# Kernel tuning notes

Hardware: AMD Instinct MI355X
Metric: run time of the kernel (lower is better)

The kernel has to match this reference:

```python
import jax, jax.numpy as jnp
import numpy as np

B, T, C, H, O = 256, 256, 32, 512, 32
OUT_TIME = 32


def setup_inputs() -> dict:
    key = jax.random.key(0)
    ks = jax.random.split(key, 10)
    times = jnp.arange(T, dtype=jnp.float32)
    coeffs = jax.random.normal(ks[0], (B, T, C), jnp.float32)
    final_index = jax.random.randint(ks[1], (B,), 0, T)
    dW = jax.random.normal(ks[2], (T - 1, B, H), jnp.float32)  # unit-normal; scaled by sqrt(dt) inside
    s = lambda k, shape, fan: jax.random.normal(k, shape, jnp.float32) / np.float32(np.sqrt(fan))
    return {
        "times": times, "coeffs": coeffs, "final_index": final_index, "dW": dW,
        "W_init": s(ks[3], (C, H), C), "b_init": jnp.zeros((H,), jnp.float32),
        "W1": s(ks[4], (H + C, H), H + C), "b1": jnp.zeros((H,), jnp.float32),
        "W2": s(ks[5], (H, H), H), "b2": jnp.zeros((H,), jnp.float32),
        "Wg": s(ks[6], (H, H), H), "bg": jnp.zeros((H,), jnp.float32),
        "Wh1": s(ks[7], (H, H), H), "bh1": jnp.zeros((H,), jnp.float32),
        "Wh2": s(ks[8], (H, O), H), "bh2": jnp.zeros((O,), jnp.float32),
    }


def reference(times, coeffs, final_index, dW, W_init, b_init, W1, b1, W2, b2, Wg, bg, Wh1, bh1, Wh2, bh2):
    # dt = max(min(diff(times)), 0.001)  (Euler method default in the torch module)
    dt = jnp.maximum(jnp.min(times[1:] - times[:-1]), jnp.float32(0.001))
    sqdt = jnp.sqrt(dt)

    x_seq = jnp.transpose(coeffs, (1, 0, 2))  # [T, B, C] control path at grid points
    # z0 = initial_network(X.evaluate(times[0]))
    z0 = x_seq[0] @ W_init + b_init  # [B, H]

    def step(y, inp):
        xk, dWk = inp  # [B, C], [B, H]
        h = jnp.tanh(jnp.concatenate([y, xk], axis=-1) @ W1 + b1)
        f = jnp.tanh(h @ W2 + b2)                # drift
        g = jax.nn.sigmoid(y @ Wg + bg)          # diagonal diffusion
        y_next = y + f * dt + g * (sqdt * dWk)   # Euler-Maruyama step
        return y_next, y_next

    _, zs = jax.lax.scan(step, z0, (x_seq[:-1], dW))  # zs: [T-1, B, H]
    z = jnp.concatenate([z0[None], zs], axis=0)       # [T, B, H]
    z = jnp.transpose(z, (1, 0, 2))                   # [B, T, H]  (transpose loop in torch code)
    z_tail = z[:, z.shape[1] - OUT_TIME:, :]          # last output_time steps
    return jax.nn.relu(z_tail @ Wh1 + bh1) @ Wh2 + bh2  # [B, OUT_TIME, O]
```

## Files before the change

kernel.cpp:

```cpp
#include <hip/hip_runtime.h>
#include <stdint.h>
#include <stddef.h>

typedef __attribute__((ext_vector_type(8))) short short8;
typedef __attribute__((ext_vector_type(8))) _Float16 half8;
typedef __attribute__((ext_vector_type(4))) float f32x4;
typedef unsigned long long ull;

#define T_  256
#define B_  256
#define C_  32
#define H_  512
#define O_  32
#define KB1 17
#define NT1 64
#define KB2 16
#define NT2 32

__device__ __forceinline__ short f2h(float f) {
  _Float16 h = (_Float16)f;
  return __builtin_bit_cast(short, h);
}
__device__ __forceinline__ void f2hl(float f, short& hi, short& lo) {
  _Float16 h = (_Float16)f;
  _Float16 l = (_Float16)(f - (float)h);
  hi = __builtin_bit_cast(short, h);
  lo = __builtin_bit_cast(short, l);
}
__device__ __forceinline__ unsigned int pack_hl(float f) {
  short h, l;
  f2hl(f, h, l);
  return (unsigned int)(unsigned short)h | ((unsigned int)(unsigned short)l << 16);
}
__device__ __forceinline__ float fast_tanh(float x) {
  float e = __expf(2.0f * x);
  return 1.0f - 2.0f / (e + 1.0f);
}
__device__ __forceinline__ float fast_sigmoid(float x) {
  return 1.0f / (1.0f + __expf(-x));
}
__device__ __forceinline__ f32x4 mfma16(half8 a, half8 b, f32x4 c) {
  return __builtin_amdgcn_mfma_f32_16x16x32_f16(a, b, c, 0, 0, 0);
}
__device__ __forceinline__ half8 ld8(const short* p) { return *(const half8*)p; }

__device__ __forceinline__ void st_coh(unsigned int* p, unsigned int v) {
  __hip_atomic_store(p, v, __ATOMIC_RELAXED, __HIP_MEMORY_SCOPE_AGENT);
}
__device__ __forceinline__ ull ld_coh(const ull* p) {
  return __hip_atomic_load(p, __ATOMIC_RELAXED, __HIP_MEMORY_SCOPE_AGENT);
}

__device__ __forceinline__ void stage_pl(const ull* src, short* hi, short* lo,
                                         int stride, int tid) {
  ull v[16];
  #pragma unroll
  for (int i = 0; i < 8; ++i) {
    int p = i * 256 + tid;
    v[2 * i]     = ld_coh(src + 2 * p);
    v[2 * i + 1] = ld_coh(src + 2 * p + 1);
  }
  #pragma unroll
  for (int i = 0; i < 8; ++i) {
    int p = i * 256 + tid;
    int row = p >> 7, col4 = (p & 127) << 2;
    unsigned int u0 = (unsigned int)v[2 * i],     u1 = (unsigned int)(v[2 * i] >> 32);
    unsigned int u2 = (unsigned int)v[2 * i + 1], u3 = (unsigned int)(v[2 * i + 1] >> 32);
    unsigned int hiA = (u0 & 0xffffu) | (u1 << 16);
    unsigned int hiB = (u2 & 0xffffu) | (u3 << 16);
    unsigned int loA = (u0 >> 16) | (u1 & 0xffff0000u);
    unsigned int loB = (u2 >> 16) | (u3 & 0xffff0000u);
    *(ull*)(hi + row * stride + col4) = (ull)hiA | ((ull)hiB << 32);
    *(ull*)(lo + row * stride + col4) = (ull)loA | ((ull)loB << 32);
  }
}

__device__ __forceinline__ void bg_barrier(unsigned int* cnt, unsigned int target) {
  __syncthreads();
  if (threadIdx.x == 0) {
    __hip_atomic_fetch_add(cnt, 1u, __ATOMIC_RELAXED, __HIP_MEMORY_SCOPE_AGENT);
    while (__hip_atomic_load(cnt, __ATOMIC_RELAXED, __HIP_MEMORY_SCOPE_AGENT) < target)
      __builtin_amdgcn_s_sleep(1);
  }
  __syncthreads();
}

__global__ void pack_b1s(const float* __restrict__ W1, const float* __restrict__ Wg,
                         short* __restrict__ hi, short* __restrict__ lo) {
  int gid = blockIdx.x * 256 + threadIdx.x;
  if (gid >= KB1 * NT1 * 512) return;
  int j = gid & 7, lane = (gid >> 3) & 63, tile = gid >> 9;
  int nt = tile % NT1, kb = tile / NT1;
  int k = kb * 32 + ((lane >> 4) << 3) + j;
  int n = ((nt & 31) << 4) + (lane & 15);
  float v = 0.f;
  if (nt < 32)      v = W1[k * H_ + n];
  else if (k < H_)  v = Wg[k * H_ + n];
  short h, l;
  f2hl(v, h, l);
  hi[gid] = h; lo[gid] = l;
}

__global__ void pack_s(const float* __restrict__ src, short* __restrict__ hi,
                       short* __restrict__ lo, int Ksrc, int Nsrc, int KB, int NT) {
  int gid = blockIdx.x * 256 + threadIdx.x;
  if (gid >= KB * NT * 512) return;
  int j = gid & 7, lane = (gid >> 3) & 63, tile = gid >> 9;
  int nt = tile % NT, kb = tile / NT;
  int k = kb * 32 + ((lane >> 4) << 3) + j;
  int n = (nt << 4) + (lane & 15);
  float v = (k < Ksrc && n < Nsrc) ? src[k * Nsrc + n] : 0.f;
  short h, l;
  f2hl(v, h, l);
  hi[gid] = h;
  if (lo) lo[gid] = l;
}

__global__ __launch_bounds__(256, 1) void sde_kernel(
    const float* __restrict__ times, const float* __restrict__ coeffs,
    const float* __restrict__ dW,
    const float* __restrict__ b_init, const float* __restrict__ b1,
    const float* __restrict__ b2, const float* __restrict__ bgb,
    const short* __restrict__ B1h, const short* __restrict__ B1l,
    const short* __restrict__ W2h, const short* __restrict__ W2l,
    const short* __restrict__ WIh, const short* __restrict__ WIl,
    unsigned int* __restrict__ y_pk, unsigned int* __restrict__ h_pk,
    short* __restrict__ zt, unsigned int* __restrict__ cnt_base) {
  __shared__ short yx_hi[16][552];
  __shared__ short yx_lo[16][552];
  __shared__ short hh_hi[16][520];
  __shared__ short hh_lo[16][520];
  __shared__ float g_x[16][32];
  __shared__ float redbuf[4];

  const int tid = threadIdx.x;
  const int w = tid >> 6, l = tid & 63;
  const int ra = l & 15, kq = l >> 4;
  const int bid = blockIdx.x;
  const int bg = bid & 15, cg = bid >> 4;
  const int R0 = bg << 4;
  unsigned int* cnt = cnt_base + bg * 32;

  const int nt1w = (w < 2) ? (2 * cg + w) : (32 + 2 * cg + (w - 2));
  const int extcol = nt1w * 16 + ra;
  const int ntF = 2 * cg + (w & 1);
  const int fcol = ntF * 16 + ra;

  float d = 1e30f;
  if (tid < T_ - 1) d = times[tid + 1] - times[tid];
  #pragma unroll
  for (int s = 32; s >= 1; s >>= 1) d = fminf(d, __shfl_xor(d, s, 64));
  if (l == 0) redbuf[w] = d;

  half8 wb1h[17], wb1l[17];
  #pragma unroll
  for (int kb = 0; kb < 17; ++kb) {
    const size_t off = ((size_t)(kb * 64 + nt1w) << 9) + (l << 3);
    wb1h[kb] = ld8(B1h + off);
    wb1l[kb] = ld8(B1l + off);
  }
  half8 ww2h[16], ww2l[16];
  if (w < 2) {
    #pragma unroll
    for (int kb = 0; kb < 16; ++kb) {
      const size_t off = ((size_t)(kb * 32 + ntF) << 9) + (l << 3);
      ww2h[kb] = ld8(W2h + off);
      ww2l[kb] = ld8(W2l + off);
    }
  }

  if (tid < 64) {
    int row = tid >> 2, cc = (tid & 3) << 3;
    const float* xb = coeffs + (size_t)(R0 + row) * (T_ * C_) + cc;
    short8 hi, lo;
    #pragma unroll
    for (int j = 0; j < 8; ++j) {
      short h, l2;
      f2hl(xb[j], h, l2);
      hi[j] = h; lo[j] = l2;
    }
    *(short8*)&yx_hi[row][512 + cc] = hi;
    *(short8*)&yx_lo[row][512 + cc] = lo;
  }
  __syncthreads();
  float m = fminf(fminf(redbuf[0], redbuf[1]), fminf(redbuf[2], redbuf[3]));
  const float dt = fmaxf(m, 0.001f);
  const float sq = sqrtf(dt);

  const float b1v = (w < 2) ? b1[extcol] : 0.f;
  const float bgv = (w >= 2) ? bgb[extcol - 512] : 0.f;
  const float b2v = (w < 2) ? b2[fcol] : 0.f;

  float yr[4] = {0.f, 0.f, 0.f, 0.f};
  if (w < 2) {
    half8 ah = ld8(&yx_hi[ra][512 + (kq << 3)]);
    half8 al = ld8(&yx_lo[ra][512 + (kq << 3)]);
    half8 bh = ld8(WIh + ((size_t)ntF << 9) + (l << 3));
    half8 bl = ld8(WIl + ((size_t)ntF << 9) + (l << 3));
    f32x4 Z = {0.f, 0.f, 0.f, 0.f};
    Z = mfma16(ah, bh, Z); Z = mfma16(al, bh, Z); Z = mfma16(ah, bl, Z);
    float bi = b_init[fcol];
    #pragma unroll
    for (int r = 0; r < 4; ++r) {
      yr[r] = Z[r] + bi;
      st_coh(&y_pk[(size_t)(R0 + (kq << 2) + r) * H_ + fcol], pack_hl(yr[r]));
    }
  }
  bg_barrier(cnt, 16u);

  for (int k = 0; k < T_ - 1; ++k) {
    float dwv[4];
    if (w < 2) {
      const float* dwb = dW + ((size_t)k * B_ + R0) * H_ + fcol;
      #pragma unroll
      for (int r = 0; r < 4; ++r)
        dwv[r] = __builtin_nontemporal_load(dwb + ((kq << 2) + r) * H_);
    }
    stage_pl((const ull*)y_pk + R0 * 256, &yx_hi[0][0], &yx_lo[0][0], 552, tid);
    __syncthreads();
    f32x4 Aa = {0.f, 0.f, 0.f, 0.f}, Ab = Aa, Ac = Aa;
    #pragma unroll
    for (int kb = 0; kb < 17; ++kb) {
      half8 ah = ld8(&yx_hi[ra][(kb << 5) + (kq << 3)]);
      half8 al = ld8(&yx_lo[ra][(kb << 5) + (kq << 3)]);
      Aa = mfma16(ah, wb1h[kb], Aa);
      Ab = mfma16(al, wb1h[kb], Ab);
      Ac = mfma16(ah, wb1l[kb], Ac);
    }
    if (w < 2) {
      #pragma unroll
      for (int r = 0; r < 4; ++r) {
        float h = fast_tanh((Aa[r] + Ab[r]) + Ac[r] + b1v);
        st_coh(&h_pk[(size_t)(R0 + (kq << 2) + r) * H_ + extcol], pack_hl(h));
      }
    } else {
      #pragma unroll
      for (int r = 0; r < 4; ++r)
        g_x[(kq << 2) + r][((w - 2) << 4) + ra] =
            fast_sigmoid((Aa[r] + Ab[r]) + Ac[r] + bgv);
    }
    bg_barrier(cnt, 16u * (2u * (unsigned)k + 2u));
    stage_pl((const ull*)h_pk + R0 * 256, &hh_hi[0][0], &hh_lo[0][0], 520, tid);
    __syncthreads();
    if (w < 2) {
      f32x4 Fa = {0.f, 0.f, 0.f, 0.f}, Fb = Fa, Fc = Fa;
      #pragma unroll
      for (int kb = 0; kb < 16; ++kb) {
        half8 ah = ld8(&hh_hi[ra][(kb << 5) + (kq << 3)]);
        half8 al = ld8(&hh_lo[ra][(kb << 5) + (kq << 3)]);
        Fa = mfma16(ah, ww2h[kb], Fa);
        Fb = mfma16(al, ww2h[kb], Fb);
        Fc = mfma16(ah, ww2l[kb], Fc);
      }
      #pragma unroll
      for (int r = 0; r < 4; ++r) {
        float f = fast_tanh((Fa[r] + Fb[r]) + Fc[r] + b2v);
        float g = g_x[(kq << 2) + r][((w & 1) << 4) + ra];
        yr[r] += f * dt + g * (sq * dwv[r]);
        st_coh(&y_pk[(size_t)(R0 + (kq << 2) + r) * H_ + fcol], pack_hl(yr[r]));
      }
      if (k >= T_ - 1 - O_) {
        int t = k - (T_ - 1 - O_);
        #pragma unroll
        for (int r = 0; r < 4; ++r)
          zt[((size_t)(R0 + (kq << 2) + r) * O_ + t) * H_ + fcol] = f2h(yr[r]);
      }
    } else if (w == 2 && k < T_ - 2) {
      int row = l >> 2, cc = (l & 3) << 3;
      const float* xb =
          coeffs + (size_t)(R0 + row) * (T_ * C_) + (size_t)(k + 1) * C_ + cc;
      short8 hi, lo;
      #pragma unroll
      for (int j = 0; j < 8; ++j) {
        short h, l2;
        f2hl(xb[j], h, l2);
        hi[j] = h; lo[j] = l2;
      }
      *(short8*)&yx_hi[row][512 + cc] = hi;
      *(short8*)&yx_lo[row][512 + cc] = lo;
    }
    bg_barrier(cnt, 16u * (2u * (unsigned)k + 3u));
  }
}

__global__ __launch_bounds__(256) void head_kernel(
    const short* __restrict__ zt, const short* __restrict__ Wh1p,
    const short* __restrict__ Wh2p, const float* __restrict__ bh1,
    const float* __restrict__ bh2, float* __restrict__ out) {
  __shared__ short a_lds[32][520];
  __shared__ short h2_lds[32][520];
  const int tid = threadIdx.x;
  const int w = tid >> 6, l = tid & 63;
  const int ra = l & 15, kq = l >> 4;
  const int r0 = blockIdx.x << 5;

  const short* zb = zt + (size_t)r0 * H_;
  #pragma unroll
  for (int i = 0; i < 8; ++i) {
    int cidx = i * 256 + tid;
    int row = cidx >> 6, cc = (cidx & 63) << 3;
    *(short8*)&a_lds[row][cc] = *(const short8*)(zb + row * H_ + cc);
  }
  __syncthreads();

  f32x4 acc[2][8];
  #pragma unroll
  for (int mt = 0; mt < 2; ++mt)
    #pragma unroll
    for (int i = 0; i < 8; ++i) acc[mt][i] = (f32x4){0.f, 0.f, 0.f, 0.f};
  for (int kb = 0; kb < 16; ++kb) {
    half8 a0 = ld8(&a_lds[ra][(kb << 5) + (kq << 3)]);
    half8 a1 = ld8(&a_lds[16 + ra][(kb << 5) + (kq << 3)]);
    const short* bp = Wh1p + (size_t)kb * (32 * 512) + (l << 3);
    #pragma unroll
    for (int i = 0; i < 8; ++i) {
      half8 b = ld8(bp + ((8 * w + i) << 9));
      acc[0][i] = mfma16(a0, b, acc[0][i]);
      acc[1][i] = mfma16(a1, b, acc[1][i]);
    }
  }
  #pragma unroll
  for (int i = 0; i < 8; ++i) {
    int col = ((8 * w + i) << 4) + ra;
    float bb = bh1[col];
    #pragma unroll
    for (int mt = 0; mt < 2; ++mt)
      #pragma unroll
      for (int r = 0; r < 4; ++r) {
        float h = acc[mt][i][r] + bb;
        h = h > 0.f ? h : 0.f;
        h2_lds[(mt << 4) + (kq << 2) + r][col] = f2h(h);
      }
  }
  __syncthreads();

  {
    int mt = w >> 1, nt = w & 1;
    f32x4 F = {0.f, 0.f, 0.f, 0.f};
    for (int kb = 0; kb < 16; ++kb) {
      half8 a = ld8(&h2_lds[(mt << 4) + ra][(kb << 5) + (kq << 3)]);
      half8 b = ld8(Wh2p + (size_t)((kb * 2 + nt) * 64 + l) * 8);
      F = mfma16(a, b, F);
    }
    int col = (nt << 4) + ra;
    float bb = bh2[col];
    #pragma unroll
    for (int r = 0; r < 4; ++r)
      out[(size_t)(r0 + (mt << 4) + (kq << 2) + r) * O_ + col] = F[r] + bb;
  }
}

extern "C" void kernel_launch(void* const* d_in, const int* in_sizes, int n_in,
                              void* d_out, int out_size, void* d_ws, size_t ws_size,
                              hipStream_t stream) {
  (void)in_sizes; (void)n_in; (void)out_size; (void)ws_size;
  const float* times  = (const float*)d_in[0];
  const float* coeffs = (const float*)d_in[1];
  const float* dW     = (const float*)d_in[3];
  const float* W_init = (const float*)d_in[4];
  const float* b_init = (const float*)d_in[5];
  const float* W1     = (const float*)d_in[6];
  const float* b1     = (const float*)d_in[7];
  const float* W2     = (const float*)d_in[8];
  const float* b2     = (const float*)d_in[9];
  const float* Wg     = (const float*)d_in[10];
  const float* bg     = (const float*)d_in[11];
  const float* Wh1    = (const float*)d_in[12];
  const float* bh1    = (const float*)d_in[13];
  const float* Wh2    = (const float*)d_in[14];
  const float* bh2    = (const float*)d_in[15];
  float* out = (float*)d_out;
  char* ws = (char*)d_ws;

  short* B1h  = (short*)(ws + 0);
  short* B1l  = (short*)(ws + 1114112);
  short* W2h  = (short*)(ws + 2228224);
  short* W2l  = (short*)(ws + 2752512);
  short* WIh  = (short*)(ws + 3276800);
  short* WIl  = (short*)(ws + 3309568);
  short* Wh1p = (short*)(ws + 3342336);
  short* Wh2p = (short*)(ws + 3866624);
  unsigned int* y_pk = (unsigned int*)(ws + 3899392);
  unsigned int* h_pk = (unsigned int*)(ws + 4423680);
  short* zt   = (short*)(ws + 4947968);
  unsigned int* cnt = (unsigned int*)(ws + 13336576);

  pack_b1s<<<2176, 256, 0, stream>>>(W1, Wg, B1h, B1l);
  pack_s  <<<1024, 256, 0, stream>>>(W2, W2h, W2l, 512, 512, 16, 32);
  pack_s  <<<64,   256, 0, stream>>>(W_init, WIh, WIl, 32, 512, 1, 32);
  pack_s  <<<1024, 256, 0, stream>>>(Wh1, Wh1p, (short*)nullptr, 512, 512, 16, 32);
  pack_s  <<<64,   256, 0, stream>>>(Wh2, Wh2p, (short*)nullptr, 512, 32, 16, 2);

  hipMemsetAsync(ws + 13336576, 0, 2048, stream);

  sde_kernel<<<256, 256, 0, stream>>>(times, coeffs, dW, b_init, b1, b2, bg,
                                      B1h, B1l, W2h, W2l, WIh, WIl,
                                      y_pk, h_pk, zt, cnt);
  head_kernel<<<256, 256, 0, stream>>>(zt, Wh1p, Wh2p, bh1, bh2, out);
}
```

Before: 1.511 ms.

## Replace batch-group barriers with split counters and staged partial waits

Swaps the single 16-block counter barrier per batch group for four counters, each covering four column blocks. A block now waits only on the pair of counters whose y or h columns it needs next, then stages that half and runs the matching half of the MFMA K loop. Work on the first half can start before all producers finish, overlapping synchronisation with compute, and the arrive step no longer spins. The catch is more polling of atomics, extra __syncthreads, and a counter-ordering scheme whose correctness depends on the relaxed atomics behaving as expected; reuse of the coeffs/LDS buffers across steps also relies on the new wait placement.

Result: slower. 2.656 ms (+75.8%).

```diff
diff --git a/kernel.cpp b/kernel.cpp
--- a/kernel.cpp
+++ b/kernel.cpp
@@ -51,38 +51,38 @@
   return __hip_atomic_load(p, __ATOMIC_RELAXED, __HIP_MEMORY_SCOPE_AGENT);
 }
 
-__device__ __forceinline__ void stage_pl(const ull* src, short* hi, short* lo,
-                                         int stride, int tid) {
-  ull v[16];
-  #pragma unroll
-  for (int i = 0; i < 8; ++i) {
-    int p = i * 256 + tid;
-    v[2 * i]     = ld_coh(src + 2 * p);
-    v[2 * i + 1] = ld_coh(src + 2 * p + 1);
-  }
-  #pragma unroll
-  for (int i = 0; i < 8; ++i) {
-    int p = i * 256 + tid;
-    int row = p >> 7, col4 = (p & 127) << 2;
-    unsigned int u0 = (unsigned int)v[2 * i],     u1 = (unsigned int)(v[2 * i] >> 32);
-    unsigned int u2 = (unsigned int)v[2 * i + 1], u3 = (unsigned int)(v[2 * i + 1] >> 32);
-    unsigned int hiA = (u0 & 0xffffu) | (u1 << 16);
-    unsigned int hiB = (u2 & 0xffffu) | (u3 << 16);
-    unsigned int loA = (u0 >> 16) | (u1 & 0xffff0000u);
-    unsigned int loB = (u2 >> 16) | (u3 & 0xffff0000u);
-    *(ull*)(hi + row * stride + col4) = (ull)hiA | ((ull)hiB << 32);
-    *(ull*)(lo + row * stride + col4) = (ull)loA | ((ull)loB << 32);
-  }
-}
-
-__device__ __forceinline__ void bg_barrier(unsigned int* cnt, unsigned int target) {
-  __syncthreads();
-  if (threadIdx.x == 0) {
-    __hip_atomic_fetch_add(cnt, 1u, __ATOMIC_RELAXED, __HIP_MEMORY_SCOPE_AGENT);
-    while (__hip_atomic_load(cnt, __ATOMIC_RELAXED, __HIP_MEMORY_SCOPE_AGENT) < target)
-      __builtin_amdgcn_s_sleep(1);
-  }
-  __syncthreads();
+__device__ __forceinline__ void pair_wait(const unsigned int* cnt_bg, int pairIdx,
+                                          unsigned int target) {
+  const unsigned int* p = cnt_bg + (size_t)((pairIdx << 1) | (threadIdx.x & 1)) * 32;
+  while (!__all((int)(__hip_atomic_load(p, __ATOMIC_RELAXED,
+                                        __HIP_MEMORY_SCOPE_AGENT) >= target)))
+    __builtin_amdgcn_s_sleep(1);
+  __builtin_amdgcn_sched_barrier(0);
+  asm volatile("" ::: "memory");
+}
+
+__device__ __forceinline__ void stage_grp(const unsigned int* src_pk, int R0, int g,
+                                          short* hi, short* lo, int stride, int tid) {
+  int row = tid >> 4;
+  int c0 = ((tid & 15) << 3) + (g << 7);
+  const ull* s = (const ull*)(src_pk + (size_t)(R0 + row) * H_ + c0);
+  ull v0 = ld_coh(s), v1 = ld_coh(s + 1), v2 = ld_coh(s + 2), v3 = ld_coh(s + 3);
+  unsigned int u0 = (unsigned int)v0, u1 = (unsigned int)(v0 >> 32);
+  unsigned int u2 = (unsigned int)v1, u3 = (unsigned int)(v1 >> 32);
+  unsigned int u4 = (unsigned int)v2, u5 = (unsigned int)(v2 >> 32);
+  unsigned int u6 = (unsigned int)v3, u7 = (unsigned int)(v3 >> 32);
+  ull hiA = (ull)((u0 & 0xffffu) | (u1 << 16)) |
+            ((ull)((u2 & 0xffffu) | (u3 << 16)) << 32);
+  ull hiB = (ull)((u4 & 0xffffu) | (u5 << 16)) |
+            ((ull)((u6 & 0xffffu) | (u7 << 16)) << 32);
+  ull loA = (ull)((u0 >> 16) | (u1 & 0xffff0000u)) |
+            ((ull)((u2 >> 16) | (u3 & 0xffff0000u)) << 32);
+  ull loB = (ull)((u4 >> 16) | (u5 & 0xffff0000u)) |
+            ((ull)((u6 >> 16) | (u7 & 0xffff0000u)) << 32);
+  *(ull*)(hi + row * stride + c0)     = hiA;
+  *(ull*)(hi + row * stride + c0 + 4) = hiB;
+  *(ull*)(lo + row * stride + c0)     = loA;
+  *(ull*)(lo + row * stride + c0 + 4) = loB;
 }
 
 __global__ void pack_b1s(const float* __restrict__ W1, const float* __restrict__ Wg,
@@ -139,7 +139,8 @@
   const int bid = blockIdx.x;
   const int bg = bid & 15, cg = bid >> 4;
   const int R0 = bg << 4;
-  unsigned int* cnt = cnt_base + bg * 32;
+  unsigned int* cnt_bg = cnt_base + (bg << 2) * 32;
+  unsigned int* myCnt  = cnt_bg + (cg >> 2) * 32;
 
   const int nt1w = (w < 2) ? (2 * cg + w) : (32 + 2 * cg + (w - 2));
   const int extcol = nt1w * 16 + ra;
@@ -206,9 +207,14 @@
       st_coh(&y_pk[(size_t)(R0 + (kq << 2) + r) * H_ + fcol], pack_hl(yr[r]));
     }
   }
-  bg_barrier(cnt, 16u);
+  __syncthreads();
+  if (tid == 0)
+    __hip_atomic_fetch_add(myCnt, 1u, __ATOMIC_RELAXED, __HIP_MEMORY_SCOPE_AGENT);
 
   for (int k = 0; k < T_ - 1; ++k) {
+    const unsigned int tgtY = 4u * (2u * (unsigned)k + 1u);
+    const unsigned int tgtH = 4u * (2u * (unsigned)k + 2u);
+
     float dwv[4];
     if (w < 2) {
       const float* dwb = dW + ((size_t)k * B_ + R0) * H_ + fcol;
@@ -216,17 +222,32 @@
       for (int r = 0; r < 4; ++r)
         dwv[r] = __builtin_nontemporal_load(dwb + ((kq << 2) + r) * H_);
     }
-    stage_pl((const ull*)y_pk + R0 * 256, &yx_hi[0][0], &yx_lo[0][0], 552, tid);
+
+    pair_wait(cnt_bg, 0, tgtY);
+    stage_grp(y_pk, R0, 0, &yx_hi[0][0], &yx_lo[0][0], 552, tid);
+    stage_grp(y_pk, R0, 1, &yx_hi[0][0], &yx_lo[0][0], 552, tid);
     __syncthreads();
     f32x4 Aa = {0.f, 0.f, 0.f, 0.f}, Ab = Aa, Ac = Aa;
     #pragma unroll
-    for (int kb = 0; kb < 17; ++kb) {
+    for (int kb = 0; kb < 8; ++kb) {
       half8 ah = ld8(&yx_hi[ra][(kb << 5) + (kq << 3)]);
       half8 al = ld8(&yx_lo[ra][(kb << 5) + (kq << 3)]);
       Aa = mfma16(ah, wb1h[kb], Aa);
       Ab = mfma16(al, wb1h[kb], Ab);
       Ac = mfma16(ah, wb1l[kb], Ac);
     }
+    pair_wait(cnt_bg, 1, tgtY);
+    stage_grp(y_pk, R0, 2, &yx_hi[0][0], &yx_lo[0][0], 552, tid);
+    stage_grp(y_pk, R0, 3, &yx_hi[0][0], &yx_lo[0][0], 552, tid);
+    __syncthreads();
+    #pragma unroll
+    for (int kb = 8; kb < 17; ++kb) {
+      half8 ah = ld8(&yx_hi[ra][(kb << 5) + (kq << 3)]);
+      half8 al = ld8(&yx_lo[ra][(kb << 5) + (kq << 3)]);
+      Aa = mfma16(ah, wb1h[kb], Aa);
+      Ab = mfma16(al, wb1h[kb], Ab);
+      Ac = mfma16(ah, wb1l[kb], Ac);
+    }
     if (w < 2) {
       #pragma unroll
       for (int r = 0; r < 4; ++r) {
@@ -239,19 +260,51 @@
         g_x[(kq << 2) + r][((w - 2) << 4) + ra] =
             fast_sigmoid((Aa[r] + Ab[r]) + Ac[r] + bgv);
     }
-    bg_barrier(cnt, 16u * (2u * (unsigned)k + 2u));
-    stage_pl((const ull*)h_pk + R0 * 256, &hh_hi[0][0], &hh_lo[0][0], 520, tid);
-    __syncthreads();
+    __syncthreads();
+    if (tid == 0)
+      __hip_atomic_fetch_add(myCnt, 1u, __ATOMIC_RELAXED, __HIP_MEMORY_SCOPE_AGENT);
+
+    pair_wait(cnt_bg, 0, tgtH);
+    stage_grp(h_pk, R0, 0, &hh_hi[0][0], &hh_lo[0][0], 520, tid);
+    stage_grp(h_pk, R0, 1, &hh_hi[0][0], &hh_lo[0][0], 520, tid);
+    __syncthreads();
+    f32x4 Fa = {0.f, 0.f, 0.f, 0.f}, Fb = Fa, Fc = Fa;
     if (w < 2) {
-      f32x4 Fa = {0.f, 0.f, 0.f, 0.f}, Fb = Fa, Fc = Fa;
-      #pragma unroll
-      for (int kb = 0; kb < 16; ++kb) {
+      #pragma unroll
+      for (int kb = 0; kb < 8; ++kb) {
         half8 ah = ld8(&hh_hi[ra][(kb << 5) + (kq << 3)]);
         half8 al = ld8(&hh_lo[ra][(kb << 5) + (kq << 3)]);
         Fa = mfma16(ah, ww2h[kb], Fa);
         Fb = mfma16(al, ww2h[kb], Fb);
         Fc = mfma16(ah, ww2l[kb], Fc);
       }
+    } else if (w == 2 && k < T_ - 2) {
+      int row = l >> 2, cc = (l & 3) << 3;
+      const float* xb =
+          coeffs + (size_t)(R0 + row) * (T_ * C_) + (size_t)(k + 1) * C_ + cc;
+      short8 hi, lo;
+      #pragma unroll
+      for (int j = 0; j < 8; ++j) {
+        short h, l2;
+        f2hl(xb[j], h, l2);
+        hi[j] = h; lo[j] = l2;
+      }
+      *(short8*)&yx_hi[row][512 + cc] = hi;
+      *(short8*)&yx_lo[row][512 + cc] = lo;
+    }
+    pair_wait(cnt_bg, 1, tgtH);
+    stage_grp(h_pk, R0, 2, &hh_hi[0][0], &hh_lo[0][0], 520, tid);
+    stage_grp(h_pk, R0, 3, &hh_hi[0][0], &hh_lo[0][0], 520, tid);
+    __syncthreads();
+    if (w < 2) {
+      #pragma unroll
+      for (int kb = 8; kb < 16; ++kb) {
+        half8 ah = ld8(&hh_hi[ra][(kb << 5) + (kq << 3)]);
+        half8 al = ld8(&hh_lo[ra][(kb << 5) + (kq << 3)]);
+        Fa = mfma16(ah, ww2h[kb], Fa);
+        Fb = mfma16(al, ww2h[kb], Fb);
+        Fc = mfma16(ah, ww2l[kb], Fc);
+      }
       #pragma unroll
       for (int r = 0; r < 4; ++r) {
         float f = fast_tanh((Fa[r] + Fb[r]) + Fc[r] + b2v);
@@ -265,21 +318,10 @@
         for (int r = 0; r < 4; ++r)
           zt[((size_t)(R0 + (kq << 2) + r) * O_ + t) * H_ + fcol] = f2h(yr[r]);
       }
-    } else if (w == 2 && k < T_ - 2) {
-      int row = l >> 2, cc = (l & 3) << 3;
-      const float* xb =
-          coeffs + (size_t)(R0 + row) * (T_ * C_) + (size_t)(k + 1) * C_ + cc;
-      short8 hi, lo;
-      #pragma unroll
-      for (int j = 0; j < 8; ++j) {
-        short h, l2;
-        f2hl(xb[j], h, l2);
-        hi[j] = h; lo[j] = l2;
-      }
-      *(short8*)&yx_hi[row][512 + cc] = hi;
-      *(short8*)&yx_lo[row][512 + cc] = lo;
-    }
-    bg_barrier(cnt, 16u * (2u * (unsigned)k + 3u));
+    }
+    __syncthreads();
+    if (tid == 0)
+      __hip_atomic_fetch_add(myCnt, 1u, __ATOMIC_RELAXED, __HIP_MEMORY_SCOPE_AGENT);
   }
 }
 
@@ -391,7 +433,7 @@
   pack_s  <<<1024, 256, 0, stream>>>(Wh1, Wh1p, (short*)nullptr, 512, 512, 16, 32);
   pack_s  <<<64,   256, 0, stream>>>(Wh2, Wh2p, (short*)nullptr, 512, 32, 16, 2);
 
-  hipMemsetAsync(ws + 13336576, 0, 2048, stream);
+  hipMemsetAsync(ws + 13336576, 0, 8192, stream);
 
   sde_kernel<<<256, 256, 0, stream>>>(times, coeffs, dW, b_init, b1, b2, bg,
                                       B1h, B1l, W2h, W2l, WIh, WIl,
```
